# Kernel tuning notes

Measured on AMD Instinct MI355X. Metric: run time of the kernel, lower is better.

Reference implementation:

```python
import jax, jax.numpy as jnp
import numpy as np

N_NODES = 50000
N_EDGES = 800000
N_GRAPHS = 512
IN_CH = 7
HID = 128
FC = 128
N_CLASSES = 2
NEG_SLOPE = 0.2


def setup_inputs() -> dict:
    key = jax.random.key(0)
    ks = jax.random.split(key, 20)
    x = jax.random.normal(ks[0], (N_NODES, IN_CH), dtype=jnp.float32)
    edge_index = jax.random.randint(ks[1], (2, N_EDGES), 0, N_NODES, dtype=jnp.int64)
    batch = jnp.sort(jax.random.randint(ks[2], (N_NODES,), 0, N_GRAPHS, dtype=jnp.int64))
    inp = {"x": x, "edge_index": edge_index, "batch": batch}
    dims = [(IN_CH, HID), (HID, HID), (HID, HID)]
    for l, (din, dout) in enumerate(dims):
        inp[f"W{l}"] = jax.random.normal(ks[3 + 4 * l], (din, dout), dtype=jnp.float32) * (1.0 / np.sqrt(din))
        inp[f"a_src{l}"] = jax.random.normal(ks[4 + 4 * l], (dout,), dtype=jnp.float32) * 0.1
        inp[f"a_dst{l}"] = jax.random.normal(ks[5 + 4 * l], (dout,), dtype=jnp.float32) * 0.1
        inp[f"b{l}"] = jnp.zeros((dout,), dtype=jnp.float32)
    inp["fc1_w"] = jax.random.normal(ks[15], (HID, FC), dtype=jnp.float32) * (1.0 / np.sqrt(HID))
    inp["fc1_b"] = jnp.zeros((FC,), dtype=jnp.float32)
    inp["fc2_w"] = jax.random.normal(ks[16], (FC, N_CLASSES), dtype=jnp.float32) * (1.0 / np.sqrt(FC))
    inp["fc2_b"] = jnp.zeros((N_CLASSES,), dtype=jnp.float32)
    return inp


def _gat_conv(x, src, dst, W, a_s, a_d, b):
    # x: [N, din] -> h: [N, dout]
    h = x @ W
    alpha_src = h @ a_s  # [N]
    alpha_dst = h @ a_d  # [N]
    e = alpha_src[src] + alpha_dst[dst]  # [E]
    e = jnp.where(e > 0, e, NEG_SLOPE * e)  # LeakyReLU(0.2)
    # segment softmax over destination node neighborhoods
    m = jax.ops.segment_max(e, dst, num_segments=N_NODES)
    m = jnp.where(jnp.isfinite(m), m, 0.0)
    e = jnp.exp(e - m[dst])
    s = jax.ops.segment_sum(e, dst, num_segments=N_NODES)
    alpha = e / (s[dst] + 1e-16)  # [E]
    out = jax.ops.segment_sum(alpha[:, None] * h[src], dst, num_segments=N_NODES)
    return out + b


def _forward(x, edge_index, batch, params):
    # PyG GATConv default: add self-loops
    loop = jnp.arange(N_NODES, dtype=edge_index.dtype)
    src = jnp.concatenate([edge_index[0], loop])
    dst = jnp.concatenate([edge_index[1], loop])
    for l in range(3):
        W, a_s, a_d, b = params[f"W{l}"], params[f"a_src{l}"], params[f"a_dst{l}"], params[f"b{l}"]
        x = jax.nn.elu(_gat_conv(x, src, dst, W, a_s, a_d, b))
    # global mean pool over graphs
    sums = jax.ops.segment_sum(x, batch, num_segments=N_GRAPHS)  # [G, HID]
    cnt = jax.ops.segment_sum(jnp.ones((N_NODES,), x.dtype), batch, num_segments=N_GRAPHS)
    g = sums / jnp.maximum(cnt, 1.0)[:, None]
    h = jax.nn.relu(g @ params["fc1_w"] + params["fc1_b"])
    logits = h @ params["fc2_w"] + params["fc2_b"]
    return jax.nn.log_softmax(logits, axis=1)


def reference(x, edge_index, batch, W0, a_src0, a_dst0, b0, W1, a_src1, a_dst1, b1,
              W2, a_src2, a_dst2, b2, fc1_w, fc1_b, fc2_w, fc2_b):
    params = {"W0": W0, "a_src0": a_src0, "a_dst0": a_dst0, "b0": b0,
              "W1": W1, "a_src1": a_src1, "a_dst1": a_dst1, "b1": b1,
              "W2": W2, "a_src2": a_src2, "a_dst2": a_dst2, "b2": b2,
              "fc1_w": fc1_w, "fc1_b": fc1_b, "fc2_w": fc2_w, "fc2_b": fc2_b}
    return _forward(x, edge_index, batch, params)
```

## Files before the change

### kernel.cpp

```cpp
#include <hip/hip_runtime.h>
#include <math.h>

#define N_NODES 50000
#define N_EDGES 800000
#define N_GRAPHS 512
#define IN_CH 7
#define HID 128
#define FC 128
#define ET (N_EDGES + N_NODES)
#define NEG_SLOPE 0.2f


__global__ void k_init_deg(int* __restrict__ deg) {
  int i = blockIdx.x * blockDim.x + threadIdx.x;
  if (i < N_NODES) deg[i] = 1;
}

__global__ void k_hist(const int* __restrict__ dst, int* __restrict__ deg) {
  int i = blockIdx.x * blockDim.x + threadIdx.x;
  if (i < N_EDGES) atomicAdd(&deg[dst[i]], 1);
}

__global__ __launch_bounds__(1024) void k_scan(const int* __restrict__ deg,
                                               int* __restrict__ row_start,
                                               int* __restrict__ cursor) {
  __shared__ int wsum[16];
  __shared__ int s_carry;
  int tid = threadIdx.x;
  int lane = tid & 63, wid = tid >> 6;
  if (tid == 0) s_carry = 0;
  __syncthreads();
  for (int base = 0; base < N_NODES; base += 1024) {
    int i = base + tid;
    int v = (i < N_NODES) ? deg[i] : 0;
    int inc = v;
    #pragma unroll
    for (int off = 1; off < 64; off <<= 1) {
      int t = __shfl_up(inc, off, 64);
      if (lane >= off) inc += t;
    }
    if (lane == 63) wsum[wid] = inc;
    __syncthreads();
    if (wid == 0) {
      int wv = (lane < 16) ? wsum[lane] : 0;
      #pragma unroll
      for (int off = 1; off < 16; off <<= 1) {
        int t = __shfl_up(wv, off, 64);
        if (lane >= off) wv += t;
      }
      if (lane < 16) wsum[lane] = wv;
    }
    __syncthreads();
    int woff = (wid > 0) ? wsum[wid - 1] : 0;
    int incl = s_carry + woff + inc;
    int excl = incl - v;
    if (i < N_NODES) { row_start[i] = excl; cursor[i] = excl; }
    __syncthreads();
    if (tid == 1023) s_carry += wsum[15];
    __syncthreads();
  }
  if (tid == 0) row_start[N_NODES] = s_carry;
}

__global__ void k_fill(const int* __restrict__ esrc, const int* __restrict__ edst,
                       int* __restrict__ cursor, int* __restrict__ csr_src) {
  int i = blockIdx.x * blockDim.x + threadIdx.x;
  if (i < ET) {
    int s, d;
    if (i < N_EDGES) { s = esrc[i]; d = edst[i]; }
    else             { s = d = i - N_EDGES; }
    int pos = atomicAdd(&cursor[d], 1);
    csr_src[pos] = s;
  }
}

__global__ void k_zero(float* __restrict__ p, int n) {
  int i = blockIdx.x * blockDim.x + threadIdx.x;
  if (i < n) p[i] = 0.f;
}


template<int DIN, int NPB>
__global__ __launch_bounds__(128) void k_gemm_small(const float* __restrict__ x,
                                                    const float* __restrict__ W,
                                                    const float* __restrict__ a_s,
                                                    const float* __restrict__ a_d,
                                                    float* __restrict__ h,
                                                    float* __restrict__ as_,
                                                    float* __restrict__ ad_) {
  __shared__ float Ws[DIN * HID];
  __shared__ float xs[DIN];
  __shared__ float red[4];
  int tid = threadIdx.x;
  for (int i = tid; i < DIN * HID; i += 128) Ws[i] = W[i];
  float asf = a_s[tid], adf = a_d[tid];
  int node0 = blockIdx.x * NPB;
  for (int nn = 0; nn < NPB; ++nn) {
    int node = node0 + nn;
    if (node >= N_NODES) break;
    __syncthreads();
    if (tid < DIN) xs[tid] = x[(size_t)node * DIN + tid];
    __syncthreads();
    float acc = 0.f;
    #pragma unroll
    for (int k = 0; k < DIN; ++k) acc = fmaf(xs[k], Ws[k * HID + tid], acc);
    h[(size_t)node * HID + tid] = acc;
    float vs = acc * asf, vd = acc * adf;
    #pragma unroll
    for (int off = 32; off >= 1; off >>= 1) {
      vs += __shfl_xor(vs, off, 64);
      vd += __shfl_xor(vd, off, 64);
    }
    int lane = tid & 63, wid = tid >> 6;
    if (lane == 0) { red[wid * 2] = vs; red[wid * 2 + 1] = vd; }
    __syncthreads();
    if (tid == 0)      as_[node] = red[0] + red[2];
    else if (tid == 1) ad_[node] = red[1] + red[3];
  }
}


#define TM 64
#define TN 64

__global__ __launch_bounds__(256, 2) void k_gemm128(const float* __restrict__ x,
                                                    const float* __restrict__ W,
                                                    const float* __restrict__ a_s,
                                                    const float* __restrict__ a_d,
                                                    float* __restrict__ h,
                                                    float* __restrict__ as_,
                                                    float* __restrict__ ad_) {
  __shared__ float xT[HID][TM + 4];
  __shared__ float Wl[HID][TN + 4];
  int tid = threadIdx.x;
  int node0 = blockIdx.x * TM;
  int col0  = blockIdx.y * TN;

  {
    const float4* xg = (const float4*)x;
    #pragma unroll
    for (int it = 0; it < (TM * 32) / 256; ++it) {
      int idx = tid + it * 256;
      int r = idx >> 5, k4 = idx & 31;
      int node = node0 + r;
      float4 v = make_float4(0.f, 0.f, 0.f, 0.f);
      if (node < N_NODES) v = xg[(size_t)node * 32 + k4];
      xT[4 * k4 + 0][r] = v.x;
      xT[4 * k4 + 1][r] = v.y;
      xT[4 * k4 + 2][r] = v.z;
      xT[4 * k4 + 3][r] = v.w;
    }
  }
  {
    const float4* wg = (const float4*)W;
    #pragma unroll
    for (int it = 0; it < (HID * (TN / 4)) / 256; ++it) {
      int idx = tid + it * 256;
      int k = idx >> 4, c4 = idx & 15;
      float4 v = wg[(size_t)k * 32 + (col0 >> 2) + c4];
      *(float4*)&Wl[k][4 * c4] = v;
    }
  }
  __syncthreads();

  int cg = tid & 15;
  int nr = tid >> 4;
  float acc00 = 0.f, acc01 = 0.f, acc02 = 0.f, acc03 = 0.f;
  float acc10 = 0.f, acc11 = 0.f, acc12 = 0.f, acc13 = 0.f;
  float acc20 = 0.f, acc21 = 0.f, acc22 = 0.f, acc23 = 0.f;
  float acc30 = 0.f, acc31 = 0.f, acc32 = 0.f, acc33 = 0.f;

  #pragma unroll 8
  for (int k = 0; k < HID; ++k) {
    float4 xv = *(const float4*)&xT[k][nr * 4];
    float4 wv = *(const float4*)&Wl[k][cg * 4];
    acc00 = fmaf(xv.x, wv.x, acc00); acc01 = fmaf(xv.x, wv.y, acc01);
    acc02 = fmaf(xv.x, wv.z, acc02); acc03 = fmaf(xv.x, wv.w, acc03);
    acc10 = fmaf(xv.y, wv.x, acc10); acc11 = fmaf(xv.y, wv.y, acc11);
    acc12 = fmaf(xv.y, wv.z, acc12); acc13 = fmaf(xv.y, wv.w, acc13);
    acc20 = fmaf(xv.z, wv.x, acc20); acc21 = fmaf(xv.z, wv.y, acc21);
    acc22 = fmaf(xv.z, wv.z, acc22); acc23 = fmaf(xv.z, wv.w, acc23);
    acc30 = fmaf(xv.w, wv.x, acc30); acc31 = fmaf(xv.w, wv.y, acc31);
    acc32 = fmaf(xv.w, wv.z, acc32); acc33 = fmaf(xv.w, wv.w, acc33);
  }

  float as0 = a_s[col0 + 4 * cg + 0], as1 = a_s[col0 + 4 * cg + 1];
  float as2 = a_s[col0 + 4 * cg + 2], as3 = a_s[col0 + 4 * cg + 3];
  float ad0 = a_d[col0 + 4 * cg + 0], ad1 = a_d[col0 + 4 * cg + 1];
  float ad2 = a_d[col0 + 4 * cg + 2], ad3 = a_d[col0 + 4 * cg + 3];

  #pragma unroll
  for (int i = 0; i < 4; ++i) {
    float r0 = (i == 0) ? acc00 : (i == 1) ? acc10 : (i == 2) ? acc20 : acc30;
    float r1 = (i == 0) ? acc01 : (i == 1) ? acc11 : (i == 2) ? acc21 : acc31;
    float r2 = (i == 0) ? acc02 : (i == 1) ? acc12 : (i == 2) ? acc22 : acc32;
    float r3 = (i == 0) ? acc03 : (i == 1) ? acc13 : (i == 2) ? acc23 : acc33;
    int node = node0 + nr * 4 + i;
    float ps = fmaf(r0, as0, fmaf(r1, as1, fmaf(r2, as2, r3 * as3)));
    float pd = fmaf(r0, ad0, fmaf(r1, ad1, fmaf(r2, ad2, r3 * ad3)));
    #pragma unroll
    for (int off = 1; off < 16; off <<= 1) {
      ps += __shfl_xor(ps, off, 16);
      pd += __shfl_xor(pd, off, 16);
    }
    if (node < N_NODES) {
      float4 hv; hv.x = r0; hv.y = r1; hv.z = r2; hv.w = r3;
      *(float4*)&h[(size_t)node * HID + col0 + 4 * cg] = hv;
      if (cg == 0) {
        atomicAdd(&as_[node], ps);
        atomicAdd(&ad_[node], pd);
      }
    }
  }
}


__global__ __launch_bounds__(256) void k_agg(const float* __restrict__ h,
                                             const float* __restrict__ as_,
                                             const float* __restrict__ ad_,
                                             const int* __restrict__ row_start,
                                             const int* __restrict__ csr_src,
                                             const float* __restrict__ b,
                                             float* __restrict__ out) {
  int wid = threadIdx.x >> 6, lane = threadIdx.x & 63;
  int node = blockIdx.x * 4 + wid;
  if (node >= N_NODES) return;
  int beg = row_start[node], end = row_start[node + 1];
  int n = end - beg;
  float adn = ad_[node];
  const float2* h2 = (const float2*)h;
  float a0 = 0.f, a1 = 0.f, c0 = 0.f, c1 = 0.f;
  float inv;

  if (n <= 64) {
    int sc_l = csr_src[beg + (lane < n ? lane : n - 1)];
    float e = as_[sc_l] + adn;
    e = e > 0.f ? e : NEG_SLOPE * e;
    float m = (lane < n) ? e : -INFINITY;
    #pragma unroll
    for (int off = 32; off >= 1; off >>= 1) m = fmaxf(m, __shfl_xor(m, off, 64));
    float we = (lane < n) ? __expf(e - m) : 0.f;
    float s = we;
    #pragma unroll
    for (int off = 32; off >= 1; off >>= 1) s += __shfl_xor(s, off, 64);
    inv = 1.f / (s + 1e-16f);
    int wbits = __float_as_int(we);

    int j = 0;
    for (; j + 4 <= n; j += 4) {
      int s0 = __builtin_amdgcn_readlane(sc_l, j);
      int s1 = __builtin_amdgcn_readlane(sc_l, j + 1);
      int s2 = __builtin_amdgcn_readlane(sc_l, j + 2);
      int s3 = __builtin_amdgcn_readlane(sc_l, j + 3);
      float w0 = __int_as_float(__builtin_amdgcn_readlane(wbits, j));
      float w1 = __int_as_float(__builtin_amdgcn_readlane(wbits, j + 1));
      float w2 = __int_as_float(__builtin_amdgcn_readlane(wbits, j + 2));
      float w3 = __int_as_float(__builtin_amdgcn_readlane(wbits, j + 3));
      float2 h0 = h2[(size_t)s0 * 64 + lane];
      float2 h1 = h2[(size_t)s1 * 64 + lane];
      float2 hh2 = h2[(size_t)s2 * 64 + lane];
      float2 h3 = h2[(size_t)s3 * 64 + lane];
      a0 = fmaf(w0, h0.x, a0);  a1 = fmaf(w0, h0.y, a1);
      c0 = fmaf(w1, h1.x, c0);  c1 = fmaf(w1, h1.y, c1);
      a0 = fmaf(w2, hh2.x, a0); a1 = fmaf(w2, hh2.y, a1);
      c0 = fmaf(w3, h3.x, c0);  c1 = fmaf(w3, h3.y, c1);
    }
    for (; j < n; ++j) {
      int sj = __builtin_amdgcn_readlane(sc_l, j);
      float wj = __int_as_float(__builtin_amdgcn_readlane(wbits, j));
      float2 hv = h2[(size_t)sj * 64 + lane];
      a0 = fmaf(wj, hv.x, a0);  a1 = fmaf(wj, hv.y, a1);
    }
  } else {
    float m = -INFINITY;
    for (int i = beg + lane; i < end; i += 64) {
      float e = as_[csr_src[i]] + adn;
      e = e > 0.f ? e : NEG_SLOPE * e;
      m = fmaxf(m, e);
    }
    #pragma unroll
    for (int off = 32; off >= 1; off >>= 1) m = fmaxf(m, __shfl_xor(m, off, 64));
    float s = 0.f;
    for (int i = beg; i < end; ++i) {
      int sc = csr_src[i];
      float e = as_[sc] + adn;
      e = e > 0.f ? e : NEG_SLOPE * e;
      float w = __expf(e - m);
      s += w;
      float2 hv = h2[(size_t)sc * 64 + lane];
      a0 = fmaf(w, hv.x, a0);
      a1 = fmaf(w, hv.y, a1);
    }
    inv = 1.f / (s + 1e-16f);
  }

  float2 bv = ((const float2*)b)[lane];
  float v0 = (a0 + c0) * inv + bv.x;
  float v1 = (a1 + c1) * inv + bv.y;
  v0 = v0 > 0.f ? v0 : expm1f(v0);
  v1 = v1 > 0.f ? v1 : expm1f(v1);
  float2 ov; ov.x = v0; ov.y = v1;
  ((float2*)out)[(size_t)node * 64 + lane] = ov;
}


__global__ __launch_bounds__(128) void k_pool_mlp(const float* __restrict__ x,
                                                  const int* __restrict__ batch,
                                                  const float* __restrict__ fc1_w,
                                                  const float* __restrict__ fc1_b,
                                                  const float* __restrict__ fc2_w,
                                                  const float* __restrict__ fc2_b,
                                                  float* __restrict__ out) {
  __shared__ float g[HID];
  __shared__ float h1[HID];
  __shared__ float lgs[2];
  int gid = blockIdx.x, tid = threadIdx.x;
  int a = 0, bnd = N_NODES;
  while (a < bnd) { int mid = (a + bnd) >> 1; if (batch[mid] < gid) a = mid + 1; else bnd = mid; }
  int lo = a;
  bnd = N_NODES;
  while (a < bnd) { int mid = (a + bnd) >> 1; if (batch[mid] < gid + 1) a = mid + 1; else bnd = mid; }
  int hi = a;
  float acc = 0.f;
  for (int n = lo; n < hi; ++n) acc += x[(size_t)n * HID + tid];
  float cnt = (float)(hi - lo);
  g[tid] = acc / fmaxf(cnt, 1.f);
  __syncthreads();
  float a1 = fc1_b[tid];
  #pragma unroll 8
  for (int k = 0; k < HID; ++k) a1 = fmaf(g[k], fc1_w[k * FC + tid], a1);
  a1 = fmaxf(a1, 0.f);
  h1[tid] = a1;
  __syncthreads();
  int lane = tid & 63, w = tid >> 6;
  float p = h1[lane] * fc2_w[lane * 2 + w] + h1[64 + lane] * fc2_w[(64 + lane) * 2 + w];
  #pragma unroll
  for (int off = 32; off >= 1; off >>= 1) p += __shfl_xor(p, off, 64);
  if (lane == 0) lgs[w] = p + fc2_b[w];
  __syncthreads();
  if (tid == 0) {
    float l0 = lgs[0], l1 = lgs[1];
    float mx = fmaxf(l0, l1);
    float lse = mx + logf(expf(l0 - mx) + expf(l1 - mx));
    out[gid * 2 + 0] = l0 - lse;
    out[gid * 2 + 1] = l1 - lse;
  }
}


extern "C" void kernel_launch(void* const* d_in, const int* in_sizes, int n_in,
                              void* d_out, int out_size, void* d_ws, size_t ws_size,
                              hipStream_t stream) {
  const float* x_in  = (const float*)d_in[0];
  const int*   eidx  = (const int*)d_in[1];
  const int*   batch = (const int*)d_in[2];
  const float* W0 = (const float*)d_in[3];
  const float* aS0 = (const float*)d_in[4];
  const float* aD0 = (const float*)d_in[5];
  const float* b0 = (const float*)d_in[6];
  const float* W1 = (const float*)d_in[7];
  const float* aS1 = (const float*)d_in[8];
  const float* aD1 = (const float*)d_in[9];
  const float* b1 = (const float*)d_in[10];
  const float* W2 = (const float*)d_in[11];
  const float* aS2 = (const float*)d_in[12];
  const float* aD2 = (const float*)d_in[13];
  const float* b2 = (const float*)d_in[14];
  const float* fc1_w = (const float*)d_in[15];
  const float* fc1_b = (const float*)d_in[16];
  const float* fc2_w = (const float*)d_in[17];
  const float* fc2_b = (const float*)d_in[18];
  float* out = (float*)d_out;

  char* ws = (char*)d_ws;
  float* h   = (float*)ws;  ws += (size_t)N_NODES * HID * sizeof(float);
  float* xb  = (float*)ws;  ws += (size_t)N_NODES * HID * sizeof(float);
  float* as_ = (float*)ws;  ws += (size_t)N_NODES * sizeof(float);
  float* ad_ = (float*)ws;  ws += (size_t)N_NODES * sizeof(float);
  int* row_start = (int*)ws; ws += (size_t)(N_NODES + 1) * sizeof(int);
  int* cursor    = (int*)ws; ws += (size_t)N_NODES * sizeof(int);
  int* deg       = (int*)ws; ws += (size_t)N_NODES * sizeof(int);
  int* csr_src   = (int*)ws; ws += (size_t)ET * sizeof(int);

  const int* esrc = eidx;
  const int* edst = eidx + N_EDGES;

  k_init_deg<<<(N_NODES + 255) / 256, 256, 0, stream>>>(deg);
  k_hist<<<(N_EDGES + 255) / 256, 256, 0, stream>>>(edst, deg);
  k_scan<<<1, 1024, 0, stream>>>(deg, row_start, cursor);
  k_fill<<<(ET + 255) / 256, 256, 0, stream>>>(esrc, edst, cursor, csr_src);

  dim3 ggrid((N_NODES + TM - 1) / TM, HID / TN);
  int agg_grid = (N_NODES + 3) / 4;
  int zgrid = (2 * N_NODES + 255) / 256;

  k_gemm_small<IN_CH, 32><<<(N_NODES + 31) / 32, 128, 0, stream>>>(x_in, W0, aS0, aD0, h, as_, ad_);
  k_agg<<<agg_grid, 256, 0, stream>>>(h, as_, ad_, row_start, csr_src, b0, xb);
  k_zero<<<zgrid, 256, 0, stream>>>(as_, 2 * N_NODES);
  k_gemm128<<<ggrid, 256, 0, stream>>>(xb, W1, aS1, aD1, h, as_, ad_);
  k_agg<<<agg_grid, 256, 0, stream>>>(h, as_, ad_, row_start, csr_src, b1, xb);
  k_zero<<<zgrid, 256, 0, stream>>>(as_, 2 * N_NODES);
  k_gemm128<<<ggrid, 256, 0, stream>>>(xb, W2, aS2, aD2, h, as_, ad_);
  k_agg<<<agg_grid, 256, 0, stream>>>(h, as_, ad_, row_start, csr_src, b2, xb);

  k_pool_mlp<<<N_GRAPHS, 128, 0, stream>>>(xb, batch, fc1_w, fc1_b, fc2_w, fc2_b, out);
}
```

Measured before the change: 570.1 us.

## Record atomic ranks in histogram to drop fill atomics; split wave into half-wave float4 gathers

The histogram kernel now saves each edge's atomic return value as its rank, so the CSR fill computes positions as row_start plus rank with no second round of atomics. The separate cursor array goes away, and the fill writes use nontemporal stores. In aggregation, each wavefront is split into two 32-lane halves that handle alternate edges with float4 loads, then combined by a cross-half shuffle. This doubles bytes per load and edges in flight, at the cost of extra shuffles and an 800K-int rank buffer. Self-loops take slot 0 of each row because deg starts at 1 and ranks start from 1.

```diff
diff --git a/kernel.cpp b/kernel.cpp
--- a/kernel.cpp
+++ b/kernel.cpp
@@ -16,14 +16,14 @@
   if (i < N_NODES) deg[i] = 1;
 }
 
-__global__ void k_hist(const int* __restrict__ dst, int* __restrict__ deg) {
+__global__ void k_hist(const int* __restrict__ dst, int* __restrict__ deg,
+                       int* __restrict__ rank) {
   int i = blockIdx.x * blockDim.x + threadIdx.x;
-  if (i < N_EDGES) atomicAdd(&deg[dst[i]], 1);
+  if (i < N_EDGES) rank[i] = atomicAdd(&deg[dst[i]], 1);
 }
 
 __global__ __launch_bounds__(1024) void k_scan(const int* __restrict__ deg,
-                                               int* __restrict__ row_start,
-                                               int* __restrict__ cursor) {
+                                               int* __restrict__ row_start) {
   __shared__ int wsum[16];
   __shared__ int s_carry;
   int tid = threadIdx.x;
@@ -54,7 +54,7 @@
     int woff = (wid > 0) ? wsum[wid - 1] : 0;
     int incl = s_carry + woff + inc;
     int excl = incl - v;
-    if (i < N_NODES) { row_start[i] = excl; cursor[i] = excl; }
+    if (i < N_NODES) row_start[i] = excl;
     __syncthreads();
     if (tid == 1023) s_carry += wsum[15];
     __syncthreads();
@@ -63,14 +63,17 @@
 }
 
 __global__ void k_fill(const int* __restrict__ esrc, const int* __restrict__ edst,
-                       int* __restrict__ cursor, int* __restrict__ csr_src) {
+                       const int* __restrict__ rank, const int* __restrict__ row_start,
+                       int* __restrict__ csr_src) {
   int i = blockIdx.x * blockDim.x + threadIdx.x;
   if (i < ET) {
-    int s, d;
-    if (i < N_EDGES) { s = esrc[i]; d = edst[i]; }
-    else             { s = d = i - N_EDGES; }
-    int pos = atomicAdd(&cursor[d], 1);
-    csr_src[pos] = s;
+    if (i < N_EDGES) {
+      int pos = row_start[edst[i]] + rank[i];
+      __builtin_nontemporal_store(esrc[i], &csr_src[pos]);
+    } else {
+      int node = i - N_EDGES;
+      __builtin_nontemporal_store(node, &csr_src[row_start[node]]);
+    }
   }
 }
 
@@ -228,8 +231,10 @@
   int beg = row_start[node], end = row_start[node + 1];
   int n = end - beg;
   float adn = ad_[node];
-  const float2* h2 = (const float2*)h;
-  float a0 = 0.f, a1 = 0.f, c0 = 0.f, c1 = 0.f;
+  int sub = lane & 31, half = lane >> 5;
+  const float4* h4 = (const float4*)h;
+  float4 accA = make_float4(0.f, 0.f, 0.f, 0.f);
+  float4 accB = make_float4(0.f, 0.f, 0.f, 0.f);
   float inv;
 
   if (n <= 64) {
@@ -244,32 +249,38 @@
     #pragma unroll
     for (int off = 32; off >= 1; off >>= 1) s += __shfl_xor(s, off, 64);
     inv = 1.f / (s + 1e-16f);
-    int wbits = __float_as_int(we);
 
     int j = 0;
-    for (; j + 4 <= n; j += 4) {
-      int s0 = __builtin_amdgcn_readlane(sc_l, j);
-      int s1 = __builtin_amdgcn_readlane(sc_l, j + 1);
-      int s2 = __builtin_amdgcn_readlane(sc_l, j + 2);
-      int s3 = __builtin_amdgcn_readlane(sc_l, j + 3);
-      float w0 = __int_as_float(__builtin_amdgcn_readlane(wbits, j));
-      float w1 = __int_as_float(__builtin_amdgcn_readlane(wbits, j + 1));
-      float w2 = __int_as_float(__builtin_amdgcn_readlane(wbits, j + 2));
-      float w3 = __int_as_float(__builtin_amdgcn_readlane(wbits, j + 3));
-      float2 h0 = h2[(size_t)s0 * 64 + lane];
-      float2 h1 = h2[(size_t)s1 * 64 + lane];
-      float2 hh2 = h2[(size_t)s2 * 64 + lane];
-      float2 h3 = h2[(size_t)s3 * 64 + lane];
-      a0 = fmaf(w0, h0.x, a0);  a1 = fmaf(w0, h0.y, a1);
-      c0 = fmaf(w1, h1.x, c0);  c1 = fmaf(w1, h1.y, c1);
-      a0 = fmaf(w2, hh2.x, a0); a1 = fmaf(w2, hh2.y, a1);
-      c0 = fmaf(w3, h3.x, c0);  c1 = fmaf(w3, h3.y, c1);
-    }
-    for (; j < n; ++j) {
-      int sj = __builtin_amdgcn_readlane(sc_l, j);
-      float wj = __int_as_float(__builtin_amdgcn_readlane(wbits, j));
-      float2 hv = h2[(size_t)sj * 64 + lane];
-      a0 = fmaf(wj, hv.x, a0);  a1 = fmaf(wj, hv.y, a1);
+    for (; j + 8 <= n; j += 8) {
+      int e0 = j + half, e1 = j + 2 + half, e2 = j + 4 + half, e3 = j + 6 + half;
+      int s0 = __shfl(sc_l, e0, 64);
+      int s1 = __shfl(sc_l, e1, 64);
+      int s2 = __shfl(sc_l, e2, 64);
+      int s3 = __shfl(sc_l, e3, 64);
+      float w0 = __shfl(we, e0, 64);
+      float w1 = __shfl(we, e1, 64);
+      float w2 = __shfl(we, e2, 64);
+      float w3 = __shfl(we, e3, 64);
+      float4 v0 = h4[(size_t)s0 * 32 + sub];
+      float4 v1 = h4[(size_t)s1 * 32 + sub];
+      float4 v2 = h4[(size_t)s2 * 32 + sub];
+      float4 v3 = h4[(size_t)s3 * 32 + sub];
+      accA.x = fmaf(w0, v0.x, accA.x); accA.y = fmaf(w0, v0.y, accA.y);
+      accA.z = fmaf(w0, v0.z, accA.z); accA.w = fmaf(w0, v0.w, accA.w);
+      accB.x = fmaf(w1, v1.x, accB.x); accB.y = fmaf(w1, v1.y, accB.y);
+      accB.z = fmaf(w1, v1.z, accB.z); accB.w = fmaf(w1, v1.w, accB.w);
+      accA.x = fmaf(w2, v2.x, accA.x); accA.y = fmaf(w2, v2.y, accA.y);
+      accA.z = fmaf(w2, v2.z, accA.z); accA.w = fmaf(w2, v2.w, accA.w);
+      accB.x = fmaf(w3, v3.x, accB.x); accB.y = fmaf(w3, v3.y, accB.y);
+      accB.z = fmaf(w3, v3.z, accB.z); accB.w = fmaf(w3, v3.w, accB.w);
+    }
+    for (; j < n; j += 2) {
+      int ej = j + half;
+      int sj = __shfl(sc_l, ej, 64);
+      float wj = (ej < n) ? __shfl(we, ej, 64) : 0.f;
+      float4 vj = h4[(size_t)sj * 32 + sub];
+      accA.x = fmaf(wj, vj.x, accA.x); accA.y = fmaf(wj, vj.y, accA.y);
+      accA.z = fmaf(wj, vj.z, accA.z); accA.w = fmaf(wj, vj.w, accA.w);
     }
   } else {
     float m = -INFINITY;
@@ -281,26 +292,40 @@
     #pragma unroll
     for (int off = 32; off >= 1; off >>= 1) m = fmaxf(m, __shfl_xor(m, off, 64));
     float s = 0.f;
-    for (int i = beg; i < end; ++i) {
+    for (int i = beg + half; i < end; i += 2) {
       int sc = csr_src[i];
       float e = as_[sc] + adn;
       e = e > 0.f ? e : NEG_SLOPE * e;
       float w = __expf(e - m);
-      s += w;
-      float2 hv = h2[(size_t)sc * 64 + lane];
-      a0 = fmaf(w, hv.x, a0);
-      a1 = fmaf(w, hv.y, a1);
-    }
+      if (sub == 0) s += w;
+      float4 hv = h4[(size_t)sc * 32 + sub];
+      accA.x = fmaf(w, hv.x, accA.x); accA.y = fmaf(w, hv.y, accA.y);
+      accA.z = fmaf(w, hv.z, accA.z); accA.w = fmaf(w, hv.w, accA.w);
+    }
+    #pragma unroll
+    for (int off = 32; off >= 1; off >>= 1) s += __shfl_xor(s, off, 64);
     inv = 1.f / (s + 1e-16f);
   }
 
-  float2 bv = ((const float2*)b)[lane];
-  float v0 = (a0 + c0) * inv + bv.x;
-  float v1 = (a1 + c1) * inv + bv.y;
-  v0 = v0 > 0.f ? v0 : expm1f(v0);
-  v1 = v1 > 0.f ? v1 : expm1f(v1);
-  float2 ov; ov.x = v0; ov.y = v1;
-  ((float2*)out)[(size_t)node * 64 + lane] = ov;
+  accA.x += accB.x; accA.y += accB.y; accA.z += accB.z; accA.w += accB.w;
+  accA.x += __shfl_xor(accA.x, 32, 64);
+  accA.y += __shfl_xor(accA.y, 32, 64);
+  accA.z += __shfl_xor(accA.z, 32, 64);
+  accA.w += __shfl_xor(accA.w, 32, 64);
+
+  if (half == 0) {
+    float4 bv = ((const float4*)b)[sub];
+    float v0 = accA.x * inv + bv.x;
+    float v1 = accA.y * inv + bv.y;
+    float v2 = accA.z * inv + bv.z;
+    float v3 = accA.w * inv + bv.w;
+    v0 = v0 > 0.f ? v0 : expm1f(v0);
+    v1 = v1 > 0.f ? v1 : expm1f(v1);
+    v2 = v2 > 0.f ? v2 : expm1f(v2);
+    v3 = v3 > 0.f ? v3 : expm1f(v3);
+    float4 ov; ov.x = v0; ov.y = v1; ov.z = v2; ov.w = v3;
+    ((float4*)out)[(size_t)node * 32 + sub] = ov;
+  }
 }
 
 
@@ -378,17 +403,17 @@
   float* as_ = (float*)ws;  ws += (size_t)N_NODES * sizeof(float);
   float* ad_ = (float*)ws;  ws += (size_t)N_NODES * sizeof(float);
   int* row_start = (int*)ws; ws += (size_t)(N_NODES + 1) * sizeof(int);
-  int* cursor    = (int*)ws; ws += (size_t)N_NODES * sizeof(int);
   int* deg       = (int*)ws; ws += (size_t)N_NODES * sizeof(int);
+  int* rank      = (int*)ws; ws += (size_t)N_EDGES * sizeof(int);
   int* csr_src   = (int*)ws; ws += (size_t)ET * sizeof(int);
 
   const int* esrc = eidx;
   const int* edst = eidx + N_EDGES;
 
   k_init_deg<<<(N_NODES + 255) / 256, 256, 0, stream>>>(deg);
-  k_hist<<<(N_EDGES + 255) / 256, 256, 0, stream>>>(edst, deg);
-  k_scan<<<1, 1024, 0, stream>>>(deg, row_start, cursor);
-  k_fill<<<(ET + 255) / 256, 256, 0, stream>>>(esrc, edst, cursor, csr_src);
+  k_hist<<<(N_EDGES + 255) / 256, 256, 0, stream>>>(edst, deg, rank);
+  k_scan<<<1, 1024, 0, stream>>>(deg, row_start);
+  k_fill<<<(ET + 255) / 256, 256, 0, stream>>>(esrc, edst, rank, row_start, csr_src);
 
   dim3 ggrid((N_NODES + TM - 1) / TM, HID / TN);
   int agg_grid = (N_NODES + 3) / 4;
```

Measured after the change: 541.1 us. 5.1% less time.
